# Kernel tuning notes

Hardware: AMD Instinct MI355X
Metric: run time of the kernel (lower is better)

Reference implementation:

```python
import jax, jax.numpy as jnp
import numpy as np

BETA = 0.25  # commitment weight from __init__ default
K, D = 512, 64


def setup_inputs() -> dict:
    key = jax.random.key(0)
    k1, k2 = jax.random.split(key)
    latents = jax.random.normal(k1, (32, 64, 64, 64), dtype=jnp.float32)  # [B, D, H, W]
    # nn.Embedding weight initialized uniform(-1/K, 1/K)
    emb_weight = jax.random.uniform(k2, (K, D), dtype=jnp.float32, minval=-1.0 / K, maxval=1.0 / K)
    return {"latents": latents, "emb_weight": emb_weight, "validation": 1}


def reference(latents, emb_weight, validation):
    B, Dc, H, W = latents.shape
    lat = jnp.transpose(latents, (0, 2, 3, 1))          # [B, H, W, D]
    flat = lat.reshape(-1, Dc)                           # [N, D]
    # pairwise squared distances via sum-of-squares + matmul (as in source)
    dist = (jnp.sum(flat * flat, axis=1, keepdims=True)
            + jnp.sum(emb_weight * emb_weight, axis=1)
            - 2.0 * flat @ emb_weight.T)                 # [N, K]
    inds = jnp.argmin(dist, axis=1)                      # [N]
    # one_hot @ emb_weight == gather
    q = emb_weight[inds].reshape(B, H, W, Dc)            # [B, H, W, D]
    commitment_loss = jnp.mean((jax.lax.stop_gradient(q) - lat) ** 2)
    embedding_loss = jnp.mean((q - jax.lax.stop_gradient(lat)) ** 2)
    # eloss starts at 0.0 (and stays 0 in validation), so topology terms vanish
    vq_loss = commitment_loss * BETA + embedding_loss
    # straight-through estimator
    q_st = lat + jax.lax.stop_gradient(q - lat)
    return jnp.transpose(q_st, (0, 3, 1, 2)), vq_loss
```

## Files before the change

kernel.cpp:

```cpp
#include <hip/hip_runtime.h>


typedef __bf16 bf16_t;
typedef __attribute__((ext_vector_type(8))) __bf16 bf16x8;
typedef __attribute__((ext_vector_type(16))) float floatx16;
typedef __attribute__((ext_vector_type(4))) float floatx4;

namespace {
constexpr int K    = 512;
constexpr int D    = 64;
constexpr int HW   = 4096;
constexpr int NPIX = 32 * HW;
constexpr int QOUT = NPIX * D;
constexpr int ROWB = 144;
constexpr int EXT_BYTES  = K * ROWB;
constexpr int BIAS_OFF   = EXT_BYTES;
constexpr int SMEM_BYTES = EXT_BYTES + K * 4;
constexpr int SMEM_CHUNKS = SMEM_BYTES / 1024;
}

__global__ __launch_bounds__(64) void vq_prep(const float* __restrict__ emb,
                                              char* __restrict__ ws,
                                              float* __restrict__ loss) {
    int k = blockIdx.x * 64 + threadIdx.x;
    if (k == 0) *loss = 0.0f;
    if (k >= K) return;
    const float4* row = (const float4*)(emb + k * D);
    float4 v[16];
#pragma unroll
    for (int i = 0; i < 16; ++i) v[i] = row[i];
    float s = 0.0f;
#pragma unroll
    for (int i = 0; i < 16; ++i)
        s += v[i].x * v[i].x + v[i].y * v[i].y + v[i].z * v[i].z + v[i].w * v[i].w;
    bf16_t r[72];
#pragma unroll
    for (int i = 0; i < 16; ++i) {
        r[4 * i + 0] = (bf16_t)v[i].x;
        r[4 * i + 1] = (bf16_t)v[i].y;
        r[4 * i + 2] = (bf16_t)v[i].z;
        r[4 * i + 3] = (bf16_t)v[i].w;
    }
#pragma unroll
    for (int i = 64; i < 72; ++i) r[i] = (bf16_t)0.0f;
    bf16_t* dst = (bf16_t*)(ws + (size_t)k * ROWB);
#pragma unroll
    for (int i = 0; i < 9; ++i)
        ((bf16x8*)dst)[i] = *(const bf16x8*)(r + 8 * i);
    ((float*)(ws + BIAS_OFF))[k] = 1.0f - 0.5f * s;
}

__global__ __launch_bounds__(256) void vq_mfma(
    const float* __restrict__ lat,
    const float* __restrict__ emb,
    const char* __restrict__ wsrc,
    float* __restrict__ out,
    float* __restrict__ loss) {
    __shared__ char smem[SMEM_BYTES];

    const int lane = threadIdx.x & 63;
    const int wave = threadIdx.x >> 6;
    const int col  = lane & 31;
    const int half = lane >> 5;
    const unsigned h4 = (unsigned)(half << 2);

    for (int c = wave; c < SMEM_CHUNKS; c += 4) {
        __builtin_amdgcn_global_load_lds(
            (const __attribute__((address_space(1))) unsigned int*)(wsrc + c * 1024 + lane * 16),
            (__attribute__((address_space(3))) unsigned int*)(smem + c * 1024),
            16, 0, 0);
    }
    __syncthreads();

    const int w  = blockIdx.x * 4 + wave;
    const int n0 = w * 128 + 2 * col;
    const int b  = n0 >> 12;
    const int hw = n0 & (HW - 1);
    const float* latp = lat + (size_t)b * D * HW + hw;

    float2 rawA[32], rawB[32];
#pragma unroll
    for (int s = 0; s < 4; ++s)
#pragma unroll
        for (int j = 0; j < 8; ++j) {
            int d = s * 16 + half * 8 + j;
            rawA[s * 8 + j] = *(const float2*)(latp + (size_t)d * HW);
        }
#pragma unroll
    for (int s = 0; s < 4; ++s)
#pragma unroll
        for (int j = 0; j < 8; ++j) {
            int d = s * 16 + half * 8 + j;
            rawB[s * 8 + j] = *(const float2*)(latp + (size_t)d * HW + 64);
        }

    bf16x8 bfA[2][4];
    float xsqA0 = 0.0f, xsqA1 = 0.0f;
#pragma unroll
    for (int s = 0; s < 4; ++s)
#pragma unroll
        for (int j = 0; j < 8; ++j) {
            float2 v = rawA[s * 8 + j];
            bfA[0][s][j] = (bf16_t)v.x;
            bfA[1][s][j] = (bf16_t)v.y;
            xsqA0 += v.x * v.x;
            xsqA1 += v.y * v.y;
        }

    auto tloop = [&](const bf16x8 (&bf)[2][4], unsigned& best0, unsigned& best1) {
        best0 = 0u; best1 = 0u;
#pragma unroll 2
        for (int t = 0; t < 16; ++t) {
            floatx4 bi[4];
#pragma unroll
            for (int c4 = 0; c4 < 4; ++c4)
                bi[c4] = *(const floatx4*)(smem + BIAS_OFF + t * 128 + half * 16 + c4 * 32);
            floatx16 acc0, acc1;
#pragma unroll
            for (int r = 0; r < 16; ++r) {
                float bv = bi[r >> 2][r & 3];
                acc0[r] = bv;
                acc1[r] = bv;
            }
            const char* arow = smem + (size_t)(t * 32 + col) * ROWB + half * 16;
            bf16x8 af[4];
#pragma unroll
            for (int s = 0; s < 4; ++s) af[s] = *(const bf16x8*)(arow + s * 32);
#pragma unroll
            for (int s = 0; s < 4; ++s) {
                acc0 = __builtin_amdgcn_mfma_f32_32x32x16_bf16(af[s], bf[0][s], acc0, 0, 0, 0);
                acc1 = __builtin_amdgcn_mfma_f32_32x32x16_bf16(af[s], bf[1][s], acc1, 0, 0, 0);
            }
#pragma unroll
            for (int r = 0; r < 16; ++r) {
                unsigned cb = (unsigned)(t * 32 + ((r & 3) + 8 * (r >> 2))) | h4;
                unsigned c0 = (__float_as_uint(acc0[r]) & 0xFFFFFE00u) | cb;
                unsigned c1 = (__float_as_uint(acc1[r]) & 0xFFFFFE00u) | cb;
                best0 = best0 > c0 ? best0 : c0;
                best1 = best1 > c1 ? best1 : c1;
            }
        }
        unsigned o0 = (unsigned)__shfl_xor((int)best0, 32, 64);
        unsigned o1 = (unsigned)__shfl_xor((int)best1, 32, 64);
        best0 = best0 > o0 ? best0 : o0;
        best1 = best1 > o1 ? best1 : o1;
    };

    unsigned bestA0, bestA1;
    tloop(bfA, bestA0, bestA1);
    const int kA0 = (int)(bestA0 & 511u), kA1 = (int)(bestA1 & 511u);
    const float scA0 = __uint_as_float(bestA0 & 0xFFFFFE00u);
    const float scA1 = __uint_as_float(bestA1 & 0xFFFFFE00u);

    const float* eA0 = emb + kA0 * D + half * 8;
    const float* eA1 = emb + kA1 * D + half * 8;
    float4 qA0[8], qA1[8];
#pragma unroll
    for (int s = 0; s < 4; ++s) {
        qA0[2 * s]     = *(const float4*)(eA0 + s * 16);
        qA0[2 * s + 1] = *(const float4*)(eA0 + s * 16 + 4);
        qA1[2 * s]     = *(const float4*)(eA1 + s * 16);
        qA1[2 * s + 1] = *(const float4*)(eA1 + s * 16 + 4);
    }

    bf16x8 bfB[2][4];
    float xsqB0 = 0.0f, xsqB1 = 0.0f;
#pragma unroll
    for (int s = 0; s < 4; ++s)
#pragma unroll
        for (int j = 0; j < 8; ++j) {
            float2 v = rawB[s * 8 + j];
            bfB[0][s][j] = (bf16_t)v.x;
            bfB[1][s][j] = (bf16_t)v.y;
            xsqB0 += v.x * v.x;
            xsqB1 += v.y * v.y;
        }

    unsigned bestB0, bestB1;
    tloop(bfB, bestB0, bestB1);
    const int kB0 = (int)(bestB0 & 511u), kB1 = (int)(bestB1 & 511u);
    const float scB0 = __uint_as_float(bestB0 & 0xFFFFFE00u);
    const float scB1 = __uint_as_float(bestB1 & 0xFFFFFE00u);

    float* outpA = out + (size_t)b * D * HW + hw;
#pragma unroll
    for (int s = 0; s < 4; ++s)
#pragma unroll
        for (int j = 0; j < 8; ++j) {
            int d = s * 16 + half * 8 + j;
            float a = (j < 4) ? qA0[2 * s][j] : qA0[2 * s + 1][j - 4];
            float c = (j < 4) ? qA1[2 * s][j] : qA1[2 * s + 1][j - 4];
            *(float2*)(outpA + (size_t)d * HW) = make_float2(a, c);
        }

    const float* eB0 = emb + kB0 * D + half * 8;
    const float* eB1 = emb + kB1 * D + half * 8;
    float4 qB0[8], qB1[8];
#pragma unroll
    for (int s = 0; s < 4; ++s) {
        qB0[2 * s]     = *(const float4*)(eB0 + s * 16);
        qB0[2 * s + 1] = *(const float4*)(eB0 + s * 16 + 4);
        qB1[2 * s]     = *(const float4*)(eB1 + s * 16);
        qB1[2 * s + 1] = *(const float4*)(eB1 + s * 16 + 4);
    }
    float* outpB = outpA + 64;
#pragma unroll
    for (int s = 0; s < 4; ++s)
#pragma unroll
        for (int j = 0; j < 8; ++j) {
            int d = s * 16 + half * 8 + j;
            float a = (j < 4) ? qB0[2 * s][j] : qB0[2 * s + 1][j - 4];
            float c = (j < 4) ? qB1[2 * s][j] : qB1[2 * s + 1][j - 4];
            *(float2*)(outpB + (size_t)d * HW) = make_float2(a, c);
        }

    float xsqA0f = xsqA0 + __shfl_xor(xsqA0, 32, 64);
    float xsqA1f = xsqA1 + __shfl_xor(xsqA1, 32, 64);
    float xsqB0f = xsqB0 + __shfl_xor(xsqB0, 32, 64);
    float xsqB1f = xsqB1 + __shfl_xor(xsqB1, 32, 64);
    float sqtot = (xsqA0f - 2.0f * (scA0 - 1.0f)) + (xsqA1f - 2.0f * (scA1 - 1.0f))
                + (xsqB0f - 2.0f * (scB0 - 1.0f)) + (xsqB1f - 2.0f * (scB1 - 1.0f));
    sqtot *= 0.5f;

#pragma unroll
    for (int off = 32; off > 0; off >>= 1) sqtot += __shfl_down(sqtot, off, 64);
    __shared__ float part[4];
    if (lane == 0) part[wave] = sqtot;
    __syncthreads();
    if (threadIdx.x == 0) {
        float t = part[0] + part[1] + part[2] + part[3];
        atomicAdd(loss, t * (1.25f / (float)QOUT));
    }
}

extern "C" void kernel_launch(void* const* d_in, const int* in_sizes, int n_in,
                              void* d_out, int out_size, void* d_ws, size_t ws_size,
                              hipStream_t stream) {
    const float* lat = (const float*)d_in[0];
    const float* emb = (const float*)d_in[1];
    float* out       = (float*)d_out;
    float* loss      = out + QOUT;
    char* ws         = (char*)d_ws;

    vq_prep<<<K / 64, 64, 0, stream>>>(emb, ws, loss);
    vq_mfma<<<256, 256, 0, stream>>>(lat, emb, ws, out, loss);
}
```

Baseline: 102.5 us.

## Split per-wave work to 64 pixels and use 512-thread blocks

Each wave now handles 64 pixels in a single pass instead of two 64-pixel passes, and blocks grow to 8 waves, giving 256 blocks of 512 threads (8 waves each) instead of 256 blocks of 4 waves. This doubles the number of waves to raise parallelism and hide latency, and drops the second batch of raw latent registers to lower register pressure. The trade-off is that the codebook staged into LDS is reused by fewer pixels per wave and there is less in-wave overlap between the second batch's loads and the first batch's compute.

```diff
diff --git a/kernel.cpp b/kernel.cpp
--- a/kernel.cpp
+++ b/kernel.cpp
@@ -50,7 +50,7 @@
     ((float*)(ws + BIAS_OFF))[k] = 1.0f - 0.5f * s;
 }
 
-__global__ __launch_bounds__(256) void vq_mfma(
+__global__ __launch_bounds__(512) void vq_mfma(
     const float* __restrict__ lat,
     const float* __restrict__ emb,
     const char* __restrict__ wsrc,
@@ -64,7 +64,7 @@
     const int half = lane >> 5;
     const unsigned h4 = (unsigned)(half << 2);
 
-    for (int c = wave; c < SMEM_CHUNKS; c += 4) {
+    for (int c = wave; c < SMEM_CHUNKS; c += 8) {
         __builtin_amdgcn_global_load_lds(
             (const __attribute__((address_space(1))) unsigned int*)(wsrc + c * 1024 + lane * 16),
             (__attribute__((address_space(3))) unsigned int*)(smem + c * 1024),
@@ -72,163 +72,108 @@
     }
     __syncthreads();
 
-    const int w  = blockIdx.x * 4 + wave;
-    const int n0 = w * 128 + 2 * col;
+    const int w  = blockIdx.x * 8 + wave;
+    const int n0 = w * 64 + 2 * col;
     const int b  = n0 >> 12;
     const int hw = n0 & (HW - 1);
     const float* latp = lat + (size_t)b * D * HW + hw;
 
-    float2 rawA[32], rawB[32];
+    float2 raw[32];
 #pragma unroll
     for (int s = 0; s < 4; ++s)
 #pragma unroll
         for (int j = 0; j < 8; ++j) {
             int d = s * 16 + half * 8 + j;
-            rawA[s * 8 + j] = *(const float2*)(latp + (size_t)d * HW);
+            raw[s * 8 + j] = *(const float2*)(latp + (size_t)d * HW);
         }
+
+    bf16x8 bf[2][4];
+    float xsq0 = 0.0f, xsq1 = 0.0f;
 #pragma unroll
     for (int s = 0; s < 4; ++s)
 #pragma unroll
         for (int j = 0; j < 8; ++j) {
-            int d = s * 16 + half * 8 + j;
-            rawB[s * 8 + j] = *(const float2*)(latp + (size_t)d * HW + 64);
+            float2 v = raw[s * 8 + j];
+            bf[0][s][j] = (bf16_t)v.x;
+            bf[1][s][j] = (bf16_t)v.y;
+            xsq0 += v.x * v.x;
+            xsq1 += v.y * v.y;
         }
 
-    bf16x8 bfA[2][4];
-    float xsqA0 = 0.0f, xsqA1 = 0.0f;
+    unsigned best0 = 0u, best1 = 0u;
+#pragma unroll 2
+    for (int t = 0; t < 16; ++t) {
+        floatx4 bi[4];
 #pragma unroll
-    for (int s = 0; s < 4; ++s)
+        for (int c4 = 0; c4 < 4; ++c4)
+            bi[c4] = *(const floatx4*)(smem + BIAS_OFF + t * 128 + half * 16 + c4 * 32);
+        floatx16 acc0, acc1;
 #pragma unroll
-        for (int j = 0; j < 8; ++j) {
-            float2 v = rawA[s * 8 + j];
-            bfA[0][s][j] = (bf16_t)v.x;
-            bfA[1][s][j] = (bf16_t)v.y;
-            xsqA0 += v.x * v.x;
-            xsqA1 += v.y * v.y;
+        for (int r = 0; r < 16; ++r) {
+            float bv = bi[r >> 2][r & 3];
+            acc0[r] = bv;
+            acc1[r] = bv;
         }
-
-    auto tloop = [&](const bf16x8 (&bf)[2][4], unsigned& best0, unsigned& best1) {
-        best0 = 0u; best1 = 0u;
-#pragma unroll 2
-        for (int t = 0; t < 16; ++t) {
-            floatx4 bi[4];
+        const char* arow = smem + (size_t)(t * 32 + col) * ROWB + half * 16;
+        bf16x8 af[4];
 #pragma unroll
-            for (int c4 = 0; c4 < 4; ++c4)
-                bi[c4] = *(const floatx4*)(smem + BIAS_OFF + t * 128 + half * 16 + c4 * 32);
-            floatx16 acc0, acc1;
+        for (int s = 0; s < 4; ++s) af[s] = *(const bf16x8*)(arow + s * 32);
 #pragma unroll
-            for (int r = 0; r < 16; ++r) {
-                float bv = bi[r >> 2][r & 3];
-                acc0[r] = bv;
-                acc1[r] = bv;
-            }
-            const char* arow = smem + (size_t)(t * 32 + col) * ROWB + half * 16;
-            bf16x8 af[4];
+        for (int s = 0; s < 4; ++s) {
+            acc0 = __builtin_amdgcn_mfma_f32_32x32x16_bf16(af[s], bf[0][s], acc0, 0, 0, 0);
+            acc1 = __builtin_amdgcn_mfma_f32_32x32x16_bf16(af[s], bf[1][s], acc1, 0, 0, 0);
+        }
 #pragma unroll
-            for (int s = 0; s < 4; ++s) af[s] = *(const bf16x8*)(arow + s * 32);
-#pragma unroll
-            for (int s = 0; s < 4; ++s) {
-                acc0 = __builtin_amdgcn_mfma_f32_32x32x16_bf16(af[s], bf[0][s], acc0, 0, 0, 0);
-                acc1 = __builtin_amdgcn_mfma_f32_32x32x16_bf16(af[s], bf[1][s], acc1, 0, 0, 0);
-            }
-#pragma unroll
-            for (int r = 0; r < 16; ++r) {
-                unsigned cb = (unsigned)(t * 32 + ((r & 3) + 8 * (r >> 2))) | h4;
-                unsigned c0 = (__float_as_uint(acc0[r]) & 0xFFFFFE00u) | cb;
-                unsigned c1 = (__float_as_uint(acc1[r]) & 0xFFFFFE00u) | cb;
-                best0 = best0 > c0 ? best0 : c0;
-                best1 = best1 > c1 ? best1 : c1;
-            }
+        for (int r = 0; r < 16; ++r) {
+            unsigned cb = (unsigned)(t * 32 + ((r & 3) + 8 * (r >> 2))) | h4;
+            unsigned c0 = (__float_as_uint(acc0[r]) & 0xFFFFFE00u) | cb;
+            unsigned c1 = (__float_as_uint(acc1[r]) & 0xFFFFFE00u) | cb;
+            best0 = best0 > c0 ? best0 : c0;
+            best1 = best1 > c1 ? best1 : c1;
         }
+    }
+    {
         unsigned o0 = (unsigned)__shfl_xor((int)best0, 32, 64);
         unsigned o1 = (unsigned)__shfl_xor((int)best1, 32, 64);
         best0 = best0 > o0 ? best0 : o0;
         best1 = best1 > o1 ? best1 : o1;
-    };
+    }
+    const int k0 = (int)(best0 & 511u);
+    const int k1 = (int)(best1 & 511u);
+    const float sc0 = __uint_as_float(best0 & 0xFFFFFE00u);
+    const float sc1 = __uint_as_float(best1 & 0xFFFFFE00u);
 
-    unsigned bestA0, bestA1;
-    tloop(bfA, bestA0, bestA1);
-    const int kA0 = (int)(bestA0 & 511u), kA1 = (int)(bestA1 & 511u);
-    const float scA0 = __uint_as_float(bestA0 & 0xFFFFFE00u);
-    const float scA1 = __uint_as_float(bestA1 & 0xFFFFFE00u);
-
-    const float* eA0 = emb + kA0 * D + half * 8;
-    const float* eA1 = emb + kA1 * D + half * 8;
-    float4 qA0[8], qA1[8];
+    const float* e0 = emb + k0 * D + half * 8;
+    const float* e1 = emb + k1 * D + half * 8;
+    float* outp = out + (size_t)b * D * HW + hw;
 #pragma unroll
     for (int s = 0; s < 4; ++s) {
-        qA0[2 * s]     = *(const float4*)(eA0 + s * 16);
-        qA0[2 * s + 1] = *(const float4*)(eA0 + s * 16 + 4);
-        qA1[2 * s]     = *(const float4*)(eA1 + s * 16);
-        qA1[2 * s + 1] = *(const float4*)(eA1 + s * 16 + 4);
+#pragma unroll
+        for (int jh = 0; jh < 2; ++jh) {
+            float4 a0 = *(const float4*)(e0 + s * 16 + jh * 4);
+            float4 a1 = *(const float4*)(e1 + s * 16 + jh * 4);
+            int dbase = s * 16 + half * 8 + jh * 4;
+            *(float2*)(outp + (size_t)(dbase + 0) * HW) = make_float2(a0.x, a1.x);
+            *(float2*)(outp + (size_t)(dbase + 1) * HW) = make_float2(a0.y, a1.y);
+            *(float2*)(outp + (size_t)(dbase + 2) * HW) = make_float2(a0.z, a1.z);
+            *(float2*)(outp + (size_t)(dbase + 3) * HW) = make_float2(a0.w, a1.w);
+        }
     }
 
-    bf16x8 bfB[2][4];
-    float xsqB0 = 0.0f, xsqB1 = 0.0f;
-#pragma unroll
-    for (int s = 0; s < 4; ++s)
-#pragma unroll
-        for (int j = 0; j < 8; ++j) {
-            float2 v = rawB[s * 8 + j];
-            bfB[0][s][j] = (bf16_t)v.x;
-            bfB[1][s][j] = (bf16_t)v.y;
-            xsqB0 += v.x * v.x;
-            xsqB1 += v.y * v.y;
-        }
-
-    unsigned bestB0, bestB1;
-    tloop(bfB, bestB0, bestB1);
-    const int kB0 = (int)(bestB0 & 511u), kB1 = (int)(bestB1 & 511u);
-    const float scB0 = __uint_as_float(bestB0 & 0xFFFFFE00u);
-    const float scB1 = __uint_as_float(bestB1 & 0xFFFFFE00u);
-
-    float* outpA = out + (size_t)b * D * HW + hw;
-#pragma unroll
-    for (int s = 0; s < 4; ++s)
-#pragma unroll
-        for (int j = 0; j < 8; ++j) {
-            int d = s * 16 + half * 8 + j;
-            float a = (j < 4) ? qA0[2 * s][j] : qA0[2 * s + 1][j - 4];
-            float c = (j < 4) ? qA1[2 * s][j] : qA1[2 * s + 1][j - 4];
-            *(float2*)(outpA + (size_t)d * HW) = make_float2(a, c);
-        }
-
-    const float* eB0 = emb + kB0 * D + half * 8;
-    const float* eB1 = emb + kB1 * D + half * 8;
-    float4 qB0[8], qB1[8];
-#pragma unroll
-    for (int s = 0; s < 4; ++s) {
-        qB0[2 * s]     = *(const float4*)(eB0 + s * 16);
-        qB0[2 * s + 1] = *(const float4*)(eB0 + s * 16 + 4);
-        qB1[2 * s]     = *(const float4*)(eB1 + s * 16);
-        qB1[2 * s + 1] = *(const float4*)(eB1 + s * 16 + 4);
-    }
-    float* outpB = outpA + 64;
-#pragma unroll
-    for (int s = 0; s < 4; ++s)
-#pragma unroll
-        for (int j = 0; j < 8; ++j) {
-            int d = s * 16 + half * 8 + j;
-            float a = (j < 4) ? qB0[2 * s][j] : qB0[2 * s + 1][j - 4];
-            float c = (j < 4) ? qB1[2 * s][j] : qB1[2 * s + 1][j - 4];
-            *(float2*)(outpB + (size_t)d * HW) = make_float2(a, c);
-        }
-
-    float xsqA0f = xsqA0 + __shfl_xor(xsqA0, 32, 64);
-    float xsqA1f = xsqA1 + __shfl_xor(xsqA1, 32, 64);
-    float xsqB0f = xsqB0 + __shfl_xor(xsqB0, 32, 64);
-    float xsqB1f = xsqB1 + __shfl_xor(xsqB1, 32, 64);
-    float sqtot = (xsqA0f - 2.0f * (scA0 - 1.0f)) + (xsqA1f - 2.0f * (scA1 - 1.0f))
-                + (xsqB0f - 2.0f * (scB0 - 1.0f)) + (xsqB1f - 2.0f * (scB1 - 1.0f));
+    float xsq0f = xsq0 + __shfl_xor(xsq0, 32, 64);
+    float xsq1f = xsq1 + __shfl_xor(xsq1, 32, 64);
+    float sqtot = (xsq0f - 2.0f * (sc0 - 1.0f)) + (xsq1f - 2.0f * (sc1 - 1.0f));
     sqtot *= 0.5f;
 
 #pragma unroll
     for (int off = 32; off > 0; off >>= 1) sqtot += __shfl_down(sqtot, off, 64);
-    __shared__ float part[4];
+    __shared__ float part[8];
     if (lane == 0) part[wave] = sqtot;
     __syncthreads();
     if (threadIdx.x == 0) {
-        float t = part[0] + part[1] + part[2] + part[3];
+        float t = 0.0f;
+#pragma unroll
+        for (int i = 0; i < 8; ++i) t += part[i];
         atomicAdd(loss, t * (1.25f / (float)QOUT));
     }
 }
@@ -243,5 +188,5 @@
     char* ws         = (char*)d_ws;
 
     vq_prep<<<K / 64, 64, 0, stream>>>(emb, ws, loss);
-    vq_mfma<<<256, 256, 0, stream>>>(lat, emb, ws, out, loss);
+    vq_mfma<<<NPIX / 512, 512, 0, stream>>>(lat, emb, ws, out, loss);
 }
```

After: 100.4 us. 2.0% less time.
